# Performance work log

Hardware: AMD Instinct MI355X
Metric: run time of the kernel (lower is better)

Reference implementation:

```python
import jax, jax.numpy as jnp
import numpy as np

SIGMA2 = 0.01       # inlier_params[0] -> Scorer_dist sigma2
INLIER_ALPHA = 0.5  # inlier_params[-1]


def setup_inputs() -> dict:
    key = jax.random.key(0)
    k1, k2, k3 = jax.random.split(key, 3)
    B, H, N = 32, 256, 8192
    pts = jax.random.normal(k1, (B, N, 3), dtype=jnp.float32)
    target = jax.random.normal(k2, (B, 3), dtype=jnp.float32)
    sample_idx = jax.random.randint(k3, (B, H, 3), 0, N)
    return {"pts": pts, "target": target, "sample_idx": sample_idx}


def _fit_planes(pts, sample_idx):
    # gather 3 points per hypothesis: pts [B,N,3], sample_idx [B,H,3] -> [B,H,3,3]
    B = pts.shape[0]
    b_idx = jnp.arange(B)[:, None, None]
    tri = pts[b_idx, sample_idx]                     # [B,H,3pts,3coords]
    p0, p1, p2 = tri[:, :, 0], tri[:, :, 1], tri[:, :, 2]
    n = jnp.cross(p1 - p0, p2 - p0)                  # plane normal [B,H,3]
    d = -jnp.sum(n * p0, axis=-1, keepdims=True)     # plane offset [B,H,1]
    planes = jnp.concatenate([n, d], axis=-1)        # [B,H,4]
    # sample_hyp fallback: degenerate (all-zero) planes replaced by ones
    all_zero = jnp.all(planes == 0, axis=-1, keepdims=True)
    planes = jnp.where(all_zero, jnp.ones_like(planes), planes)
    # normalize all 4 components by normal norm
    norm = jnp.sqrt(jnp.sum(planes[..., :3] ** 2, axis=-1, keepdims=True))
    return planes / norm


def reference(pts, target, sample_idx):
    B = pts.shape[0]
    planes = _fit_planes(pts, sample_idx)            # [B,H,4]
    normal = planes[..., :3]
    # Scorer_dist: |n . p + d| over all points, gaussian, sum over points
    dists = jnp.abs(jnp.einsum('bhc,bnc->bhn', normal, pts) + planes[..., 3:4])
    score = jnp.sum(jnp.exp(-(dists ** 2) / (2.0 * SIGMA2)), axis=2)  # [B,H]
    # ms_euclidean loss against target normal (sign-invariant)
    t = target[:, None, :]                           # [B,1,3]
    loss = jnp.minimum(jnp.sum((normal - t) ** 2, axis=2),
                       jnp.sum((normal + t) ** 2, axis=2))            # [B,H]
    maxidx = jnp.argmax(score, axis=1)               # [B]
    top_loss = jnp.take_along_axis(loss, maxidx[:, None], axis=1)[:, 0]
    pred = jnp.take_along_axis(normal, maxidx[:, None, None], axis=1)[:, 0]
    w = jax.nn.softmax(INLIER_ALPHA * score, axis=1)
    exp_loss = jnp.sum(loss * w, axis=1)             # [B]
    return exp_loss, top_loss, pred
```

## Files before the change

### kernel.cpp

```cpp
#include <hip/hip_runtime.h>
#include <math.h>

#define BB 32
#define HH 256
#define NN 8192
#define CC 32
#define CHUNK (NN / CC)


__global__ __launch_bounds__(HH) void fit_planes_kernel(
    const float* __restrict__ pts, const float* __restrict__ target,
    const int* __restrict__ sidx, float* __restrict__ ws) {
  int b = blockIdx.x;
  int h = threadIdx.x;
  long base = ((long)b * HH + h) * 3;
  int i0 = sidx[base + 0], i1 = sidx[base + 1], i2 = sidx[base + 2];
  const float* pb = pts + (long)b * NN * 3;
  float p0x = pb[3 * i0], p0y = pb[3 * i0 + 1], p0z = pb[3 * i0 + 2];
  float p1x = pb[3 * i1], p1y = pb[3 * i1 + 1], p1z = pb[3 * i1 + 2];
  float p2x = pb[3 * i2], p2y = pb[3 * i2 + 1], p2z = pb[3 * i2 + 2];
  float v1x = p1x - p0x, v1y = p1y - p0y, v1z = p1z - p0z;
  float v2x = p2x - p0x, v2y = p2y - p0y, v2z = p2z - p0z;
  float nx = __fsub_rn(__fmul_rn(v1y, v2z), __fmul_rn(v1z, v2y));
  float ny = __fsub_rn(__fmul_rn(v1z, v2x), __fmul_rn(v1x, v2z));
  float nz = __fsub_rn(__fmul_rn(v1x, v2y), __fmul_rn(v1y, v2x));
  float d = -(__fmul_rn(nx, p0x) + __fmul_rn(ny, p0y) + __fmul_rn(nz, p0z));
  if (nx == 0.0f && ny == 0.0f && nz == 0.0f && d == 0.0f) {
    nx = 1.0f; ny = 1.0f; nz = 1.0f; d = 1.0f;
  }
  float norm = sqrtf(nx * nx + ny * ny + nz * nz);
  nx /= norm; ny /= norm; nz /= norm; d /= norm;
  ((float4*)ws)[b * HH + h] = make_float4(nx, ny, nz, d);
  float tx = target[b * 3], ty = target[b * 3 + 1], tz = target[b * 3 + 2];
  float lm = (nx - tx) * (nx - tx) + (ny - ty) * (ny - ty) + (nz - tz) * (nz - tz);
  float lp = (nx + tx) * (nx + tx) + (ny + ty) * (ny + ty) + (nz + tz) * (nz + tz);
  ws[(size_t)BB * HH * 4 + b * HH + h] = fminf(lm, lp);
}

__global__ __launch_bounds__(HH) void score_partial_kernel(
    const float* __restrict__ pts, const float* __restrict__ ws,
    float* __restrict__ partial) {
  int chunk = blockIdx.x, b = blockIdx.y;
  int h = threadIdx.x;
  __shared__ float4 sm4[CHUNK * 3 / 4];
  float* sm = (float*)sm4;
  const float* src = pts + ((long)b * NN + (long)chunk * CHUNK) * 3;
  for (int j = h; j < CHUNK * 3; j += HH) sm[j] = src[j];
  float4 pl = ((const float4*)ws)[b * HH + h];
  __syncthreads();
  const float KC = -72.13475204444817f;
  float a0 = 0.f, a1 = 0.f, a2 = 0.f, a3 = 0.f;
#pragma unroll 4
  for (int g = 0; g < CHUNK / 4; ++g) {
    float4 v0 = sm4[3 * g + 0];
    float4 v1 = sm4[3 * g + 1];
    float4 v2 = sm4[3 * g + 2];
    float t0 = fmaf(pl.x, v0.x, fmaf(pl.y, v0.y, fmaf(pl.z, v0.z, pl.w)));
    float t1 = fmaf(pl.x, v0.w, fmaf(pl.y, v1.x, fmaf(pl.z, v1.y, pl.w)));
    float t2 = fmaf(pl.x, v1.z, fmaf(pl.y, v1.w, fmaf(pl.z, v2.x, pl.w)));
    float t3 = fmaf(pl.x, v2.y, fmaf(pl.y, v2.z, fmaf(pl.z, v2.w, pl.w)));
    a0 += __builtin_amdgcn_exp2f(t0 * t0 * KC);
    a1 += __builtin_amdgcn_exp2f(t1 * t1 * KC);
    a2 += __builtin_amdgcn_exp2f(t2 * t2 * KC);
    a3 += __builtin_amdgcn_exp2f(t3 * t3 * KC);
  }
  partial[((long)b * CC + chunk) * HH + h] = (a0 + a1) + (a2 + a3);
}

__global__ __launch_bounds__(HH) void finalize_kernel(
    const float* __restrict__ ws, float* __restrict__ out) {
  int b = blockIdx.x, h = threadIdx.x;
  const float* lossArr = ws + (size_t)BB * HH * 4;
  const float* partial = ws + (size_t)BB * HH * 5;
  float s = 0.f;
#pragma unroll
  for (int c = 0; c < CC; ++c) s += partial[((long)b * CC + c) * HH + h];
  float l = lossArr[b * HH + h];

  __shared__ float sv[HH];
  __shared__ int si[HH];
  __shared__ float s1[HH];
  __shared__ float s2[HH];
  sv[h] = s; si[h] = h;
  __syncthreads();
  for (int off = HH / 2; off > 0; off >>= 1) {
    if (h < off) {
      float o = sv[h + off]; int oi = si[h + off];
      if (o > sv[h] || (o == sv[h] && oi < si[h])) { sv[h] = o; si[h] = oi; }
    }
    __syncthreads();
  }
  float m = sv[0];
  int mi = si[0];
  __syncthreads();
  const float HALF_LOG2E = 0.5f * 1.4426950408889634f;
  float wv = __builtin_amdgcn_exp2f(HALF_LOG2E * (s - m));
  s1[h] = wv; s2[h] = wv * l;
  __syncthreads();
  for (int off = HH / 2; off > 0; off >>= 1) {
    if (h < off) { s1[h] += s1[h + off]; s2[h] += s2[h + off]; }
    __syncthreads();
  }
  if (h == 0) {
    out[b] = s2[0] / s1[0];
    out[BB + b] = lossArr[b * HH + mi];
    float4 p = ((const float4*)ws)[b * HH + mi];
    out[2 * BB + b * 3 + 0] = p.x;
    out[2 * BB + b * 3 + 1] = p.y;
    out[2 * BB + b * 3 + 2] = p.z;
  }
}

extern "C" void kernel_launch(void* const* d_in, const int* in_sizes, int n_in,
                              void* d_out, int out_size, void* d_ws, size_t ws_size,
                              hipStream_t stream) {
  const float* pts = (const float*)d_in[0];
  const float* target = (const float*)d_in[1];
  const int* sidx = (const int*)d_in[2];
  float* out = (float*)d_out;
  float* ws = (float*)d_ws;
  float* partial = ws + (size_t)BB * HH * 5;

  fit_planes_kernel<<<BB, HH, 0, stream>>>(pts, target, sidx, ws);
  score_partial_kernel<<<dim3(CC, BB), HH, 0, stream>>>(pts, ws, partial);
  finalize_kernel<<<BB, HH, 0, stream>>>(ws, out);
}
```

Baseline: 27.49 us.

## Fuse plane fitting, scoring and finalize into one kernel with last-block reduction

Merges the three kernels into one. Every block recomputes all plane fits for its batch in registers and LDS, stages its point chunk with direct global-to-LDS loads, and scores 8 planes per thread over a sub-chunk. It also folds the Gaussian constant into the plane coefficients, and the last block per batch (found with an atomic counter) does the argmax and softmax reduction. This removes two launches and the workspace round trips, at the cost of redundant plane fitting in every block, a memset launch, and atomic/fence synchronisation.

```diff
diff --git a/kernel.cpp b/kernel.cpp
--- a/kernel.cpp
+++ b/kernel.cpp
@@ -6,16 +6,36 @@
 #define NN 8192
 #define CC 32
 #define CHUNK (NN / CC)
+#define P 8
+#define SUB (CHUNK / P)
 
+#define WS_PARTIAL_F 64
 
-__global__ __launch_bounds__(HH) void fit_planes_kernel(
+__global__ __launch_bounds__(HH, 4) void dsac_fused(
     const float* __restrict__ pts, const float* __restrict__ target,
-    const int* __restrict__ sidx, float* __restrict__ ws) {
-  int b = blockIdx.x;
-  int h = threadIdx.x;
-  long base = ((long)b * HH + h) * 3;
-  int i0 = sidx[base + 0], i1 = sidx[base + 1], i2 = sidx[base + 2];
-  const float* pb = pts + (long)b * NN * 3;
+    const int* __restrict__ sidx, float* __restrict__ partial,
+    int* __restrict__ cnt, float* __restrict__ out) {
+  const int chunk = blockIdx.x, b = blockIdx.y;
+  const int h = threadIdx.x;
+
+  __shared__ float4 smp[CHUNK * 3 / 4];
+  __shared__ float4 plane_lds[HH];
+  __shared__ float scorepad[HH * 9];
+  __shared__ float sv[HH];
+  __shared__ int si[HH];
+  __shared__ float s1[HH];
+  __shared__ float s2[HH];
+  __shared__ int isLast;
+
+  const float4* src4 =
+      (const float4*)(pts + ((long)b * NN + (long)chunk * CHUNK) * 3);
+  if (h < CHUNK * 3 / 4) {
+    __builtin_amdgcn_global_load_lds(src4 + h, &smp[h], 16, 0, 0);
+  }
+
+  int ibase = (b * HH + h) * 3;
+  int i0 = sidx[ibase], i1 = sidx[ibase + 1], i2 = sidx[ibase + 2];
+  const float* pb = pts + b * NN * 3;
   float p0x = pb[3 * i0], p0y = pb[3 * i0 + 1], p0z = pb[3 * i0 + 2];
   float p1x = pb[3 * i1], p1y = pb[3 * i1 + 1], p1z = pb[3 * i1 + 2];
   float p2x = pb[3 * i2], p2y = pb[3 * i2 + 1], p2z = pb[3 * i2 + 2];
@@ -30,58 +50,72 @@
   }
   float norm = sqrtf(nx * nx + ny * ny + nz * nz);
   nx /= norm; ny /= norm; nz /= norm; d /= norm;
-  ((float4*)ws)[b * HH + h] = make_float4(nx, ny, nz, d);
+  plane_lds[h] = make_float4(nx, ny, nz, d);
   float tx = target[b * 3], ty = target[b * 3 + 1], tz = target[b * 3 + 2];
   float lm = (nx - tx) * (nx - tx) + (ny - ty) * (ny - ty) + (nz - tz) * (nz - tz);
   float lp = (nx + tx) * (nx + tx) + (ny + ty) * (ny + ty) + (nz + tz) * (nz + tz);
-  ws[(size_t)BB * HH * 4 + b * HH + h] = fminf(lm, lp);
-}
+  float loss_h = fminf(lm, lp);
 
-__global__ __launch_bounds__(HH) void score_partial_kernel(
-    const float* __restrict__ pts, const float* __restrict__ ws,
-    float* __restrict__ partial) {
-  int chunk = blockIdx.x, b = blockIdx.y;
-  int h = threadIdx.x;
-  __shared__ float4 sm4[CHUNK * 3 / 4];
-  float* sm = (float*)sm4;
-  const float* src = pts + ((long)b * NN + (long)chunk * CHUNK) * 3;
-  for (int j = h; j < CHUNK * 3; j += HH) sm[j] = src[j];
-  float4 pl = ((const float4*)ws)[b * HH + h];
   __syncthreads();
-  const float KC = -72.13475204444817f;
-  float a0 = 0.f, a1 = 0.f, a2 = 0.f, a3 = 0.f;
-#pragma unroll 4
-  for (int g = 0; g < CHUNK / 4; ++g) {
-    float4 v0 = sm4[3 * g + 0];
-    float4 v1 = sm4[3 * g + 1];
-    float4 v2 = sm4[3 * g + 2];
-    float t0 = fmaf(pl.x, v0.x, fmaf(pl.y, v0.y, fmaf(pl.z, v0.z, pl.w)));
-    float t1 = fmaf(pl.x, v0.w, fmaf(pl.y, v1.x, fmaf(pl.z, v1.y, pl.w)));
-    float t2 = fmaf(pl.x, v1.z, fmaf(pl.y, v1.w, fmaf(pl.z, v2.x, pl.w)));
-    float t3 = fmaf(pl.x, v2.y, fmaf(pl.y, v2.z, fmaf(pl.z, v2.w, pl.w)));
-    a0 += __builtin_amdgcn_exp2f(t0 * t0 * KC);
-    a1 += __builtin_amdgcn_exp2f(t1 * t1 * KC);
-    a2 += __builtin_amdgcn_exp2f(t2 * t2 * KC);
-    a3 += __builtin_amdgcn_exp2f(t3 * t3 * KC);
+
+  const float SC = sqrtf(72.13475204444817f);
+  const int pid = h & 31;
+  const int s = h >> 5;
+  float4 pls[P];
+#pragma unroll
+  for (int k = 0; k < P; ++k) {
+    float4 q = plane_lds[pid + (k << 5)];
+    pls[k] = make_float4(q.x * SC, q.y * SC, q.z * SC, q.w * SC);
   }
-  partial[((long)b * CC + chunk) * HH + h] = (a0 + a1) + (a2 + a3);
-}
 
-__global__ __launch_bounds__(HH) void finalize_kernel(
-    const float* __restrict__ ws, float* __restrict__ out) {
-  int b = blockIdx.x, h = threadIdx.x;
-  const float* lossArr = ws + (size_t)BB * HH * 4;
-  const float* partial = ws + (size_t)BB * HH * 5;
-  float s = 0.f;
+  float acc[P];
 #pragma unroll
-  for (int c = 0; c < CC; ++c) s += partial[((long)b * CC + c) * HH + h];
-  float l = lossArr[b * HH + h];
+  for (int k = 0; k < P; ++k) acc[k] = 0.f;
+  const int sbase = s * (SUB * 3 / 4);
+#pragma unroll 2
+  for (int g = 0; g < SUB / 4; ++g) {
+    float4 v0 = smp[sbase + 3 * g + 0];
+    float4 v1 = smp[sbase + 3 * g + 1];
+    float4 v2 = smp[sbase + 3 * g + 2];
+#pragma unroll
+    for (int k = 0; k < P; ++k) {
+      float4 q = pls[k];
+      float t0 = fmaf(q.x, v0.x, fmaf(q.y, v0.y, fmaf(q.z, v0.z, q.w)));
+      float t1 = fmaf(q.x, v0.w, fmaf(q.y, v1.x, fmaf(q.z, v1.y, q.w)));
+      float t2 = fmaf(q.x, v1.z, fmaf(q.y, v1.w, fmaf(q.z, v2.x, q.w)));
+      float t3 = fmaf(q.x, v2.y, fmaf(q.y, v2.z, fmaf(q.z, v2.w, q.w)));
+      float e0 = __builtin_amdgcn_exp2f(-(t0 * t0));
+      float e1 = __builtin_amdgcn_exp2f(-(t1 * t1));
+      float e2 = __builtin_amdgcn_exp2f(-(t2 * t2));
+      float e3 = __builtin_amdgcn_exp2f(-(t3 * t3));
+      acc[k] += (e0 + e1) + (e2 + e3);
+    }
+  }
 
-  __shared__ float sv[HH];
-  __shared__ int si[HH];
-  __shared__ float s1[HH];
-  __shared__ float s2[HH];
-  sv[h] = s; si[h] = h;
+#pragma unroll
+  for (int k = 0; k < P; ++k) scorepad[(pid + (k << 5)) * 9 + s] = acc[k];
+  __syncthreads();
+  float rowsum = 0.f;
+#pragma unroll
+  for (int j = 0; j < P; ++j) rowsum += scorepad[h * 9 + j];
+  partial[((long)b * CC + chunk) * HH + h] = rowsum;
+
+  __threadfence();
+  __syncthreads();
+  if (h == 0) {
+    int old = atomicAdd(&cnt[b], 1);
+    isLast = (old == CC - 1) ? 1 : 0;
+  }
+  __syncthreads();
+  if (!isLast) return;
+  __threadfence();
+
+  const float* prow = partial + (long)b * CC * HH + h;
+  float score = 0.f;
+#pragma unroll
+  for (int c = 0; c < CC; ++c) score += prow[(long)c * HH];
+
+  sv[h] = score; si[h] = h;
   __syncthreads();
   for (int off = HH / 2; off > 0; off >>= 1) {
     if (h < off) {
@@ -92,22 +126,21 @@
   }
   float m = sv[0];
   int mi = si[0];
-  __syncthreads();
-  const float HALF_LOG2E = 0.5f * 1.4426950408889634f;
-  float wv = __builtin_amdgcn_exp2f(HALF_LOG2E * (s - m));
-  s1[h] = wv; s2[h] = wv * l;
+  const float HL = 0.72134752044448170f;
+  float wv = __builtin_amdgcn_exp2f(HL * (score - m));
+  s1[h] = wv; s2[h] = wv * loss_h;
   __syncthreads();
   for (int off = HH / 2; off > 0; off >>= 1) {
     if (h < off) { s1[h] += s1[h + off]; s2[h] += s2[h + off]; }
     __syncthreads();
   }
-  if (h == 0) {
-    out[b] = s2[0] / s1[0];
-    out[BB + b] = lossArr[b * HH + mi];
-    float4 p = ((const float4*)ws)[b * HH + mi];
-    out[2 * BB + b * 3 + 0] = p.x;
-    out[2 * BB + b * 3 + 1] = p.y;
-    out[2 * BB + b * 3 + 2] = p.z;
+  if (h == 0) out[b] = s2[0] / s1[0];
+  if (h == mi) {
+    out[BB + b] = loss_h;
+    float4 p = plane_lds[h];
+    out[2 * BB + 3 * b + 0] = p.x;
+    out[2 * BB + 3 * b + 1] = p.y;
+    out[2 * BB + 3 * b + 2] = p.z;
   }
 }
 
@@ -118,10 +151,9 @@
   const float* target = (const float*)d_in[1];
   const int* sidx = (const int*)d_in[2];
   float* out = (float*)d_out;
-  float* ws = (float*)d_ws;
-  float* partial = ws + (size_t)BB * HH * 5;
+  int* cnt = (int*)d_ws;
+  float* partial = (float*)d_ws + WS_PARTIAL_F;
 
-  fit_planes_kernel<<<BB, HH, 0, stream>>>(pts, target, sidx, ws);
-  score_partial_kernel<<<dim3(CC, BB), HH, 0, stream>>>(pts, ws, partial);
-  finalize_kernel<<<BB, HH, 0, stream>>>(ws, out);
+  hipMemsetAsync(d_ws, 0, 128, stream);
+  dsac_fused<<<dim3(CC, BB), HH, 0, stream>>>(pts, target, sidx, partial, cnt, out);
 }
```

Measured after the change: 105.1 us. +282.3%, slower.
